# Kernel tuning notes

Measured on AMD Instinct MI355X. Metric: run time of the kernel, lower is better.

## Reference

```python
import jax, jax.numpy as jnp
import numpy as np

NUM_STAGES = 4
NUM_CODEBOOKS = 1024  # 2**vq_bitrate_per_stage
DATA_DIM = 256
BEAM = 4
N = 4096
EPS = 1e-12


def setup_inputs() -> dict:
    key = jax.random.key(0)
    k1, k2, k3 = jax.random.split(key, 3)
    x = jax.random.normal(k1, (N, DATA_DIM), jnp.float32)
    # codebooks initialized Uniform(-1/K, 1/K) as in torch __init__
    cb = jax.random.uniform(k2, (NUM_STAGES * NUM_CODEBOOKS, DATA_DIM), jnp.float32,
                            -1.0 / NUM_CODEBOOKS, 1.0 / NUM_CODEBOOKS)
    rv = jax.random.normal(k3, (N, DATA_DIM), jnp.float32)
    return {"input_data": x, "codebooks": cb, "random_vector": rv, "train_mode": 1}


def _beam_search(x, codebooks):
    """Returns best_tuples [N, S]: per-sample global codebook indices, one per stage slot."""
    B, D = x.shape
    S, K, W = NUM_STAGES, NUM_CODEBOOKS, BEAM
    cb2 = jnp.sum(codebooks ** 2, axis=1)  # [S*K]

    def dists(q):  # [..., D] -> [..., S*K] squared euclidean
        return jnp.sum(q ** 2, axis=-1, keepdims=True) - 2.0 * (q @ codebooks.T) + cb2

    stage_of = jnp.arange(S * K) // K  # stage id of each flat codebook row

    # stage 0: top-BEAM nearest entries over all stages
    idx0 = jax.lax.top_k(-dists(x), W)[1].astype(jnp.int32)  # [B, W]
    tuples = jnp.full((B, W, S), -1, jnp.int32).at[:, :, 0].set(idx0)

    for it in range(S - 1):
        # Faithful to source: vq_and_remainder loop subtracts codebooks[tuples[:,:,it]]
        # (it+1) times (the loop passes iter_number, not i).
        c_it = codebooks[tuples[:, :, it]]                      # [B, W, D]
        remainder = x[:, None, :] - (it + 1) * c_it             # [B, W, D]
        # stages already used by each beam (mask via NaN-codebooks in source == +inf here)
        used = tuples[:, :, :it + 1] // K                       # [B, W, it+1]
        banned = (used[:, :, :, None] == jnp.arange(S)).any(axis=2)  # [B, W, S]
        d = dists(remainder)                                    # [B, W, S*K]
        d = jnp.where(banned[:, :, stage_of], jnp.inf, d)
        cand = jax.lax.top_k(-d, W)[1].astype(jnp.int32)        # [B, W, W]
        prime = jnp.repeat(tuples[:, :, None, :], W, axis=2)    # [B, W, W, S]
        prime = prime.at[:, :, :, it + 1].set(cand).reshape(B, W * W, S)
        # mse over the (it+2) filled slots
        q = jnp.sum(codebooks[prime[:, :, :it + 2]], axis=2)    # [B, W*W, D]
        mse = jnp.mean((x[:, None, :] - q) ** 2, axis=2)        # [B, W*W]
        if it < S - 2:
            sel = jax.lax.top_k(-mse, W)[1]                     # [B, W] smallest-mse beams
            tuples = jnp.take_along_axis(prime, sel[:, :, None], axis=1)
        else:
            best = jnp.argmin(mse, axis=1)                      # [B]
            return jnp.take_along_axis(prime, best[:, None, None], axis=1)[:, 0, :]


def reference(input_data, codebooks, random_vector, train_mode):
    best = _beam_search(input_data, jax.lax.stop_gradient(codebooks))  # [N, S] int32
    quantized = jnp.sum(codebooks[best], axis=1)                       # [N, D]
    # noise substitution VQ
    nh = jnp.sqrt(jnp.sum((input_data - quantized) ** 2, axis=1, keepdims=True))
    nr = jnp.sqrt(jnp.sum(random_vector ** 2, axis=1, keepdims=True))
    nsvq = input_data + (nh / nr + EPS) * random_vector
    # codebooks_used starts at zero; +=1 at unique selected indices -> usage indicator
    used = jnp.zeros(NUM_STAGES * NUM_CODEBOOKS, jnp.int32).at[best.reshape(-1)].set(1)
    used = used.reshape(NUM_STAGES, NUM_CODEBOOKS)
    if train_mode:
        return (nsvq, used)
    return (quantized, used)
```

## Files before the change

kernel.cpp:

```cpp
#include <hip/hip_runtime.h>
#include <math.h>

#define NSTAGES 4
#define NCB     1024
#define SK      4096
#define D       256
#define BEAM_W  4
#define NB      4096
#define INFF    __builtin_huge_valf()
#define RB      128
#define CBL     256
#define BK      32
#define NCBLK   (SK / CBL)

typedef unsigned long long u64;


template <typename F>
__device__ __forceinline__ float xw84(F v) {
  float r[32];
#pragma unroll
  for (int l = 0; l < 32; ++l) r[l] = v(l);
  for (int i = 32; i < 256; i += 32)
#pragma unroll
    for (int l = 0; l < 32; ++l) r[l] = __fadd_rn(r[l], v(i + l));
  float w[8];
#pragma unroll
  for (int j = 0; j < 8; ++j)
    w[j] = __fadd_rn(__fadd_rn(__fadd_rn(r[j], r[8 + j]), r[16 + j]), r[24 + j]);
  float s0 = __fadd_rn(w[0], w[4]);
  float s1 = __fadd_rn(w[1], w[5]);
  float s2 = __fadd_rn(w[2], w[6]);
  float s3 = __fadd_rn(w[3], w[7]);
  float t0 = __fadd_rn(s0, s2);
  float t1 = __fadd_rn(s1, s3);
  return __fadd_rn(t0, t1);
}

__device__ __forceinline__ void ins4u(u64 v, u64 b[4]) {
  if (v < b[3]) {
    b[3] = v;
    if (b[3] < b[2]) { u64 t = b[2]; b[2] = b[3]; b[3] = t; }
    if (b[2] < b[1]) { u64 t = b[1]; b[1] = b[2]; b[2] = t; }
    if (b[1] < b[0]) { u64 t = b[0]; b[0] = b[1]; b[1] = t; }
  }
}

__device__ __forceinline__ u64 shflx64(u64 v, int m) {
  int lo = __shfl_xor((int)(unsigned)(v & 0xFFFFFFFFULL), m, 64);
  int hi = __shfl_xor((int)(unsigned)(v >> 32), m, 64);
  return ((u64)(unsigned)hi << 32) | (u64)(unsigned)lo;
}

__global__ __launch_bounds__(256) void cb2_pw(const float* __restrict__ cb,
                                              float* __restrict__ cb2) {
  int row = blockIdx.x * 256 + threadIdx.x;
  if (row >= SK) return;
  const float* c = cb + (size_t)row * D;
  cb2[row] = xw84([&](int d) { float t = c[d]; return __fmul_rn(t, t); });
}

__global__ __launch_bounds__(256) void s0_pw(const float* __restrict__ x,
                                             float* __restrict__ Srow) {
  int row = blockIdx.x * 256 + threadIdx.x;
  if (row >= NB) return;
  const float* xr = x + (size_t)row * D;
  Srow[row] = xw84([&](int d) { float t = xr[d]; return __fmul_rn(t, t); });
}

__global__ __launch_bounds__(256) void srow_pw(const float* __restrict__ x,
                                               const float* __restrict__ cb,
                                               const int* __restrict__ tuples,
                                               int it,
                                               float* __restrict__ Srow) {
  int row = blockIdx.x * 256 + threadIdx.x;
  if (row >= NB * BEAM_W) return;
  int s = row >> 2;
  int slot = tuples[row * NSTAGES + it];
  const float* xr = x + (size_t)s * D;
  const float* cr = cb + (size_t)slot * D;
  const float mf = (float)(it + 1);
  Srow[row] = xw84([&](int d) {
    float t = __fsub_rn(xr[d], __fmul_rn(mf, cr[d]));
    return __fmul_rn(t, t);
  });
}

__global__ __launch_bounds__(256) void transpose_rem(
    const float* __restrict__ x, const float* __restrict__ cbk,
    const int* __restrict__ tuples, int it, int isStep0, int nrows,
    float* __restrict__ AT) {
  __shared__ float tile[64][65];
  const int t = threadIdx.x;
  const int r0 = blockIdx.x * 64;
  const int d0 = blockIdx.y * 64;
  const float mf = (float)(it + 1);
  {
    int r = r0 + (t & 63);
    int db = (t >> 6) * 16;
    const float* xr;
    const float* cr = nullptr;
    if (isStep0) {
      xr = x + (size_t)r * D;
    } else {
      xr = x + (size_t)(r >> 2) * D;
      cr = cbk + (size_t)tuples[r * NSTAGES + it] * D;
    }
#pragma unroll
    for (int l = 0; l < 4; ++l) {
      float4 v = *(const float4*)&xr[d0 + db + l * 4];
      if (!isStep0) {
        float4 c = *(const float4*)&cr[d0 + db + l * 4];
        v.x = __fsub_rn(v.x, __fmul_rn(mf, c.x));
        v.y = __fsub_rn(v.y, __fmul_rn(mf, c.y));
        v.z = __fsub_rn(v.z, __fmul_rn(mf, c.z));
        v.w = __fsub_rn(v.w, __fmul_rn(mf, c.w));
      }
      tile[t & 63][db + l * 4 + 0] = v.x;
      tile[t & 63][db + l * 4 + 1] = v.y;
      tile[t & 63][db + l * 4 + 2] = v.z;
      tile[t & 63][db + l * 4 + 3] = v.w;
    }
  }
  __syncthreads();
  {
    int dd = t >> 2;
    int rb = (t & 3) * 16;
    float* orow = AT + (size_t)(d0 + dd) * nrows + r0 + rb;
#pragma unroll
    for (int l = 0; l < 4; ++l) {
      float4 v = make_float4(tile[rb + l * 4 + 0][dd], tile[rb + l * 4 + 1][dd],
                             tile[rb + l * 4 + 2][dd], tile[rb + l * 4 + 3][dd]);
      *(float4*)&orow[l * 4] = v;
    }
  }
}

__global__ __launch_bounds__(256, 2) void gemm_plain(
    const float* __restrict__ AT, const float* __restrict__ BT, int nrows,
    float* __restrict__ Gout) {
  __shared__ __align__(16) float AsF[BK * 128];
  __shared__ __align__(16) float BsF[BK * 256];
  const int tid  = threadIdx.x;
  const int wv   = tid >> 6;
  const int lane = tid & 63;
  const int tx = tid & 15, ty = tid >> 4;
  const int row0 = blockIdx.y * RB;
  const int col0 = blockIdx.x * CBL;

  const float* aSrc[4];
  const float* bSrc[8];
#pragma unroll
  for (int c = 0; c < 4; ++c) {
    int f = (wv * 4 + c) * 256 + lane * 4;
    aSrc[c] = AT + (size_t)(f >> 7) * nrows + row0 + (f & 127);
  }
#pragma unroll
  for (int c = 0; c < 8; ++c) {
    int f = (wv * 8 + c) * 256 + lane * 4;
    bSrc[c] = BT + (size_t)(f >> 8) * SK + col0 + (f & 255);
  }

  float acc[8][16];
#pragma unroll
  for (int i = 0; i < 8; ++i)
#pragma unroll
    for (int j = 0; j < 16; ++j) acc[i][j] = 0.0f;

  for (int kt = 0; kt < D; kt += BK) {
#pragma unroll
    for (int c = 0; c < 4; ++c)
      __builtin_amdgcn_global_load_lds(
          (const __attribute__((address_space(1))) void*)aSrc[c],
          (__attribute__((address_space(3))) void*)(AsF + (wv * 4 + c) * 256), 16, 0, 0);
#pragma unroll
    for (int c = 0; c < 8; ++c)
      __builtin_amdgcn_global_load_lds(
          (const __attribute__((address_space(1))) void*)bSrc[c],
          (__attribute__((address_space(3))) void*)(BsF + (wv * 8 + c) * 256), 16, 0, 0);
#pragma unroll
    for (int c = 0; c < 4; ++c) aSrc[c] += (size_t)BK * nrows;
#pragma unroll
    for (int c = 0; c < 8; ++c) bSrc[c] += (size_t)BK * SK;
    __syncthreads();

#pragma unroll 8
    for (int k = 0; k < BK; ++k) {
      float a[8], b[16];
      *(float4*)&a[0]  = *(const float4*)&AsF[k * 128 + ty * 4];
      *(float4*)&a[4]  = *(const float4*)&AsF[k * 128 + 64 + ty * 4];
      *(float4*)&b[0]  = *(const float4*)&BsF[k * 256 + tx * 4];
      *(float4*)&b[4]  = *(const float4*)&BsF[k * 256 + 64 + tx * 4];
      *(float4*)&b[8]  = *(const float4*)&BsF[k * 256 + 128 + tx * 4];
      *(float4*)&b[12] = *(const float4*)&BsF[k * 256 + 192 + tx * 4];
#pragma unroll
      for (int i = 0; i < 8; ++i)
#pragma unroll
        for (int j = 0; j < 16; ++j)
          acc[i][j] = __fmaf_rn(a[i], b[j], acc[i][j]);
    }
    __syncthreads();
  }

#pragma unroll
  for (int i = 0; i < 8; ++i) {
    int lrow = (i & 3) + ((i >> 2) * 64) + ty * 4;
    float* go = Gout + (size_t)(row0 + lrow) * SK + col0;
#pragma unroll
    for (int jj = 0; jj < 4; ++jj) {
      float4 v = make_float4(acc[i][jj * 4 + 0], acc[i][jj * 4 + 1],
                             acc[i][jj * 4 + 2], acc[i][jj * 4 + 3]);
      *(float4*)&go[jj * 64 + tx * 4] = v;
    }
  }
}

__global__ __launch_bounds__(256) void beam_full(
    const float* __restrict__ XC, const float* __restrict__ G,
    const float* __restrict__ Srow0, const float* __restrict__ cb2,
    const float* __restrict__ x, const float* __restrict__ cb,
    int* __restrict__ best) {
  const int s = blockIdx.x;
  const int t = threadIdx.x;
  const int b = t >> 6, l = t & 63;
  __shared__ float xcs[SK];
  __shared__ int   tup_s[4][NSTAGES];
  __shared__ float msek[16];
  __shared__ int   primes[16][NSTAGES];

  for (int i = t; i < SK / 4; i += 256)
    *(float4*)&xcs[i * 4] = *(const float4*)&XC[(size_t)s * SK + i * 4];
  __syncthreads();

  {
    const float S0 = Srow0[s];
    u64 b4[4] = {~0ULL, ~0ULL, ~0ULL, ~0ULL};
#pragma unroll 4
    for (int i = 0; i < 16; ++i) {
      int j = (i * 64 + l) * 4;
      float4 x4 = *(const float4*)&xcs[j];
      float4 c4 = *(const float4*)&cb2[j];
      float k0 = __fadd_rn(__fsub_rn(S0, __fmul_rn(2.0f, x4.x)), c4.x);
      float k1 = __fadd_rn(__fsub_rn(S0, __fmul_rn(2.0f, x4.y)), c4.y);
      float k2 = __fadd_rn(__fsub_rn(S0, __fmul_rn(2.0f, x4.z)), c4.z);
      float k3 = __fadd_rn(__fsub_rn(S0, __fmul_rn(2.0f, x4.w)), c4.w);
      ins4u(((u64)__float_as_uint(k0) << 32) | (unsigned)(j + 0), b4);
      ins4u(((u64)__float_as_uint(k1) << 32) | (unsigned)(j + 1), b4);
      ins4u(((u64)__float_as_uint(k2) << 32) | (unsigned)(j + 2), b4);
      ins4u(((u64)__float_as_uint(k3) << 32) | (unsigned)(j + 3), b4);
    }
#pragma unroll
    for (int m = 1; m < 64; m <<= 1) {
      u64 o0 = shflx64(b4[0], m);
      u64 o1 = shflx64(b4[1], m);
      u64 o2 = shflx64(b4[2], m);
      u64 o3 = shflx64(b4[3], m);
      ins4u(o0, b4);
      ins4u(o1, b4);
      ins4u(o2, b4);
      ins4u(o3, b4);
    }
    if (l == 0) tup_s[b][0] = (int)(b4[b] & 0xFFFFFFFFULL);
  }
  __syncthreads();

  for (int it = 0; it < NSTAGES - 1; ++it) {
    const float mf = (float)(it + 1);
    const int slot = tup_s[b][it];
    int banned = 0;
    for (int a = 0; a <= it; ++a) banned |= 1 << (tup_s[b][a] >> 10);

    float S;
    {
      const int ll = l & 31;
      const float* xr = x + (size_t)s * D;
      const float* cr = cb + (size_t)slot * D;
      float tt = __fsub_rn(xr[ll], __fmul_rn(mf, cr[ll]));
      float rl = __fmul_rn(tt, tt);
      for (int i = 32; i < 256; i += 32) {
        float t2 = __fsub_rn(xr[ll + i], __fmul_rn(mf, cr[ll + i]));
        rl = __fadd_rn(rl, __fmul_rn(t2, t2));
      }
      int j = l & 7;
      float rj   = __shfl(rl, j, 64);
      float rj8  = __shfl(rl, j + 8, 64);
      float rj16 = __shfl(rl, j + 16, 64);
      float rj24 = __shfl(rl, j + 24, 64);
      float w = __fadd_rn(__fadd_rn(__fadd_rn(rj, rj8), rj16), rj24);
      float w0 = __shfl(w, 0, 64), w1 = __shfl(w, 1, 64);
      float w2 = __shfl(w, 2, 64), w3 = __shfl(w, 3, 64);
      float w4 = __shfl(w, 4, 64), w5 = __shfl(w, 5, 64);
      float w6 = __shfl(w, 6, 64), w7 = __shfl(w, 7, 64);
      float s0 = __fadd_rn(w0, w4);
      float s1 = __fadd_rn(w1, w5);
      float s2 = __fadd_rn(w2, w6);
      float s3 = __fadd_rn(w3, w7);
      float t0 = __fadd_rn(s0, s2);
      float t1 = __fadd_rn(s1, s3);
      S = __fadd_rn(t0, t1);
    }

    const float* gr = G + (size_t)slot * SK;

    u64 b4[4] = {~0ULL, ~0ULL, ~0ULL, ~0ULL};
#pragma unroll 4
    for (int i = 0; i < 16; ++i) {
      int j = (i * 64 + l) * 4;
      float4 g4 = *(const float4*)&gr[j];
      float4 x4 = *(const float4*)&xcs[j];
      float4 c4 = *(const float4*)&cb2[j];
      int ban = (banned >> (j >> 10)) & 1;
      float m0 = __fsub_rn(x4.x, __fmul_rn(mf, g4.x));
      float m1 = __fsub_rn(x4.y, __fmul_rn(mf, g4.y));
      float m2 = __fsub_rn(x4.z, __fmul_rn(mf, g4.z));
      float m3 = __fsub_rn(x4.w, __fmul_rn(mf, g4.w));
      float k0 = ban ? INFF : __fadd_rn(__fsub_rn(S, __fmul_rn(2.0f, m0)), c4.x);
      float k1 = ban ? INFF : __fadd_rn(__fsub_rn(S, __fmul_rn(2.0f, m1)), c4.y);
      float k2 = ban ? INFF : __fadd_rn(__fsub_rn(S, __fmul_rn(2.0f, m2)), c4.z);
      float k3 = ban ? INFF : __fadd_rn(__fsub_rn(S, __fmul_rn(2.0f, m3)), c4.w);
      ins4u(((u64)__float_as_uint(k0) << 32) | (unsigned)(j + 0), b4);
      ins4u(((u64)__float_as_uint(k1) << 32) | (unsigned)(j + 1), b4);
      ins4u(((u64)__float_as_uint(k2) << 32) | (unsigned)(j + 2), b4);
      ins4u(((u64)__float_as_uint(k3) << 32) | (unsigned)(j + 3), b4);
    }
#pragma unroll
    for (int m = 1; m < 64; m <<= 1) {
      u64 o0 = shflx64(b4[0], m);
      u64 o1 = shflx64(b4[1], m);
      u64 o2 = shflx64(b4[2], m);
      u64 o3 = shflx64(b4[3], m);
      ins4u(o0, b4);
      ins4u(o1, b4);
      ins4u(o2, b4);
      ins4u(o3, b4);
    }

    {
      const int L = it + 2;
#pragma unroll
      for (int pi = 0; pi < 4; ++pi) {
        const int p = b * 4 + pi;
        int tpl[NSTAGES];
        for (int a = 0; a < NSTAGES; ++a) tpl[a] = tup_s[b][a];
        tpl[it + 1] = (int)(b4[pi] & 0xFFFFFFFFULL);
        if (l == 0)
          for (int a = 0; a < NSTAGES; ++a) primes[p][a] = tpl[a];
        float v[4];
#pragma unroll
        for (int m = 0; m < 4; ++m) {
          int d = l + m * 64;
          float q = cb[(size_t)tpl[0] * D + d];
          for (int a = 1; a < L; ++a) q = __fadd_rn(q, cb[(size_t)tpl[a] * D + d]);
          float dv = __fsub_rn(x[(size_t)s * D + d], q);
          v[m] = __fmul_rn(dv, dv);
        }
        float u0 = __shfl_xor(v[0], 32, 64);
        float u1 = __shfl_xor(v[1], 32, 64);
        float u2 = __shfl_xor(v[2], 32, 64);
        float u3 = __shfl_xor(v[3], 32, 64);
        float r0 = __fadd_rn(v[0], u0);
        r0 = __fadd_rn(r0, v[1]);
        r0 = __fadd_rn(r0, u1);
        r0 = __fadd_rn(r0, v[2]);
        r0 = __fadd_rn(r0, u2);
        r0 = __fadd_rn(r0, v[3]);
        r0 = __fadd_rn(r0, u3);
        float a8  = __shfl(r0, l + 8, 64);
        float a16 = __shfl(r0, l + 16, 64);
        float a24 = __shfl(r0, l + 24, 64);
        float w = __fadd_rn(__fadd_rn(__fadd_rn(r0, a8), a16), a24);
        float w0 = __shfl(w, 0, 64), w1 = __shfl(w, 1, 64);
        float w2 = __shfl(w, 2, 64), w3 = __shfl(w, 3, 64);
        float w4 = __shfl(w, 4, 64), w5 = __shfl(w, 5, 64);
        float w6 = __shfl(w, 6, 64), w7 = __shfl(w, 7, 64);
        float s0 = __fadd_rn(w0, w4);
        float s1 = __fadd_rn(w1, w5);
        float s2 = __fadd_rn(w2, w6);
        float s3 = __fadd_rn(w3, w7);
        float t0 = __fadd_rn(s0, s2);
        float t1 = __fadd_rn(s1, s3);
        float S2 = __fadd_rn(t0, t1);
        if (l == 0) msek[p] = __fmul_rn(S2, 0.00390625f);
      }
    }
    __syncthreads();

    if (t == 0) {
      if (it < NSTAGES - 2) {
        bool taken[16] = {false};
        int  newt[BEAM_W][NSTAGES];
        for (int rr2 = 0; rr2 < BEAM_W; ++rr2) {
          int bp = -1; float bk = 0.0f;
          for (int p = 0; p < 16; ++p) {
            if (taken[p]) continue;
            if (bp < 0 || msek[p] < bk) { bk = msek[p]; bp = p; }
          }
          taken[bp] = true;
          for (int a = 0; a < NSTAGES; ++a) newt[rr2][a] = primes[bp][a];
        }
        for (int rr2 = 0; rr2 < BEAM_W; ++rr2)
          for (int a = 0; a < NSTAGES; ++a) tup_s[rr2][a] = newt[rr2][a];
      } else {
        int bp = 0; float bk = msek[0];
        for (int p = 1; p < 16; ++p)
          if (msek[p] < bk) { bk = msek[p]; bp = p; }
        for (int a = 0; a < NSTAGES; ++a) best[s * NSTAGES + a] = primes[bp][a];
      }
    }
    __syncthreads();
  }
}

__global__ __launch_bounds__(256, 2) void gemm_fused(
    const float* __restrict__ AT, const float* __restrict__ BT,
    const float* __restrict__ Srow, const float* __restrict__ cb2,
    const int* __restrict__ tuples, int it, int isStep0, int nrows,
    u64* __restrict__ pki, float* __restrict__ XCout) {
  __shared__ __align__(16) char smem[66560];
  float* AsF = (float*)smem;
  float* BsF = (float*)(smem + 16384);
  u64*   tki = (u64*)smem;
  const int tid  = threadIdx.x;
  const int wv   = tid >> 6;
  const int lane = tid & 63;
  const int tx = tid & 15, ty = tid >> 4;
  const int row0 = blockIdx.y * RB;
  const int col0 = blockIdx.x * CBL;

  const float* aSrc[4];
  const float* bSrc[8];
#pragma unroll
  for (int c = 0; c < 4; ++c) {
    int f = (wv * 4 + c) * 256 + lane * 4;
    aSrc[c] = AT + (size_t)(f >> 7) * nrows + row0 + (f & 127);
  }
#pragma unroll
  for (int c = 0; c < 8; ++c) {
    int f = (wv * 8 + c) * 256 + lane * 4;
    bSrc[c] = BT + (size_t)(f >> 8) * SK + col0 + (f & 255);
  }

  float acc[8][16];
#pragma unroll
  for (int i = 0; i < 8; ++i)
#pragma unroll
    for (int j = 0; j < 16; ++j) acc[i][j] = 0.0f;

  for (int kt = 0; kt < D; kt += BK) {
#pragma unroll
    for (int c = 0; c < 4; ++c)
      __builtin_amdgcn_global_load_lds(
          (const __attribute__((address_space(1))) void*)aSrc[c],
          (__attribute__((address_space(3))) void*)(AsF + (wv * 4 + c) * 256), 16, 0, 0);
#pragma unroll
    for (int c = 0; c < 8; ++c)
      __builtin_amdgcn_global_load_lds(
          (const __attribute__((address_space(1))) void*)bSrc[c],
          (__attribute__((address_space(3))) void*)(BsF + (wv * 8 + c) * 256), 16, 0, 0);
#pragma unroll
    for (int c = 0; c < 4; ++c) aSrc[c] += (size_t)BK * nrows;
#pragma unroll
    for (int c = 0; c < 8; ++c) bSrc[c] += (size_t)BK * SK;
    __syncthreads();

#pragma unroll 8
    for (int k = 0; k < BK; ++k) {
      float a[8], b[16];
      *(float4*)&a[0]  = *(const float4*)&AsF[k * 128 + ty * 4];
      *(float4*)&a[4]  = *(const float4*)&AsF[k * 128 + 64 + ty * 4];
      *(float4*)&b[0]  = *(const float4*)&BsF[k * 256 + tx * 4];
      *(float4*)&b[4]  = *(const float4*)&BsF[k * 256 + 64 + tx * 4];
      *(float4*)&b[8]  = *(const float4*)&BsF[k * 256 + 128 + tx * 4];
      *(float4*)&b[12] = *(const float4*)&BsF[k * 256 + 192 + tx * 4];
#pragma unroll
      for (int i = 0; i < 8; ++i)
#pragma unroll
        for (int j = 0; j < 16; ++j)
          acc[i][j] = __fmaf_rn(a[i], b[j], acc[i][j]);
    }
    __syncthreads();
  }

  if (XCout) {
#pragma unroll
    for (int i = 0; i < 8; ++i) {
      int lrow = (i & 3) + ((i >> 2) * 64) + ty * 4;
      float* xo = XCout + (size_t)(row0 + lrow) * SK + col0;
#pragma unroll
      for (int jj = 0; jj < 4; ++jj) {
        float4 v = make_float4(acc[i][jj * 4 + 0], acc[i][jj * 4 + 1],
                               acc[i][jj * 4 + 2], acc[i][jj * 4 + 3]);
        *(float4*)&xo[(jj) * 64 + tx * 4] = v;
      }
    }
  }

#pragma unroll
  for (int i = 0; i < 8; ++i) {
    int lrow = (i & 3) + ((i >> 2) * 64) + ty * 4;
    int grow = row0 + lrow;
    float S = Srow[grow];
    int banned = 0;
    if (!isStep0)
      for (int a = 0; a <= it; ++a) banned |= 1 << (tuples[grow * NSTAGES + a] >> 10);
    u64 b4[4] = {~0ULL, ~0ULL, ~0ULL, ~0ULL};
#pragma unroll
    for (int j = 0; j < 16; ++j) {
      int gcol = col0 + (j & 3) + ((j >> 2) * 64) + tx * 4;
      float key = ((banned >> (gcol >> 10)) & 1)
                      ? INFF
                      : __fadd_rn(__fsub_rn(S, __fmul_rn(2.0f, acc[i][j])), cb2[gcol]);
      ins4u(((u64)__float_as_uint(key) << 32) | (unsigned)gcol, b4);
    }
#pragma unroll
    for (int s = 0; s < 4; ++s) tki[(size_t)lrow * 65 + tx * 4 + s] = b4[s];
  }
  __syncthreads();

  if (tid < RB) {
    u64 b4[4] = {~0ULL, ~0ULL, ~0ULL, ~0ULL};
    for (int t = 0; t < 16; ++t)
#pragma unroll
      for (int s = 0; s < 4; ++s) ins4u(tki[(size_t)tid * 65 + t * 4 + s], b4);
    size_t base = ((size_t)blockIdx.x * nrows + row0 + tid) * 4;
#pragma unroll
    for (int s = 0; s < 4; ++s) pki[base + s] = b4[s];
  }
}

__global__ __launch_bounds__(256) void reduce_top4(
    const u64* __restrict__ pki, int nrows, int isStep0,
    int* __restrict__ tup, int* __restrict__ cand) {
  int r = blockIdx.x * 256 + threadIdx.x;
  if (r >= nrows) return;
  u64 b4[4] = {~0ULL, ~0ULL, ~0ULL, ~0ULL};
  for (int cblk = 0; cblk < NCBLK; ++cblk) {
    size_t base = ((size_t)cblk * nrows + r) * 4;
    ins4u(pki[base + 0], b4);
    ins4u(pki[base + 1], b4);
    ins4u(pki[base + 2], b4);
    ins4u(pki[base + 3], b4);
  }
  if (isStep0) {
#pragma unroll
    for (int s = 0; s < 4; ++s)
      tup[(r * BEAM_W + s) * NSTAGES + 0] = (int)(b4[s] & 0xFFFFFFFFULL);
  } else {
#pragma unroll
    for (int s = 0; s < 4; ++s)
      cand[r * BEAM_W + s] = (int)(b4[s] & 0xFFFFFFFFULL);
  }
}

__global__ __launch_bounds__(256) void mse_select(const float* __restrict__ x,
                                                  const float* __restrict__ cb,
                                                  const int* __restrict__ cand,
                                                  int it,
                                                  int* __restrict__ tuples,
                                                  int* __restrict__ best) {
  const int s = blockIdx.x, tid = threadIdx.x;
  const int wv = tid >> 6, lane = tid & 63;
  __shared__ float buf[4][256];
  __shared__ float rr[4][32];
  __shared__ float msek[16];
  __shared__ int   primes[16][NSTAGES];
  const int L = it + 2;

  for (int pi = 0; pi < 4; ++pi) {
    const int p = wv * 4 + pi;
    const int b = p >> 2, c = p & 3;
    int tpl[NSTAGES];
    for (int a = 0; a < NSTAGES; ++a) tpl[a] = tuples[(s * BEAM_W + b) * NSTAGES + a];
    tpl[it + 1] = cand[(s * BEAM_W + b) * BEAM_W + c];
    if (lane == 0)
      for (int a = 0; a < NSTAGES; ++a) primes[p][a] = tpl[a];
    for (int d = lane; d < D; d += 64) {
      float q = cb[(size_t)tpl[0] * D + d];
      for (int a = 1; a < L; ++a) q = __fadd_rn(q, cb[(size_t)tpl[a] * D + d]);
      float v = __fsub_rn(x[(size_t)s * D + d], q);
      buf[wv][d] = __fmul_rn(v, v);
    }
    __syncthreads();
    if (lane < 32) {
      float r = buf[wv][lane];
      for (int i = 32; i < 256; i += 32) r = __fadd_rn(r, buf[wv][i + lane]);
      rr[wv][lane] = r;
    }
    __syncthreads();
    if (lane == 0) {
      float w[8];
#pragma unroll
      for (int j = 0; j < 8; ++j)
        w[j] = __fadd_rn(__fadd_rn(__fadd_rn(rr[wv][j], rr[wv][8 + j]), rr[wv][16 + j]),
                         rr[wv][24 + j]);
      float s0 = __fadd_rn(w[0], w[4]);
      float s1 = __fadd_rn(w[1], w[5]);
      float s2 = __fadd_rn(w[2], w[6]);
      float s3 = __fadd_rn(w[3], w[7]);
      float t0 = __fadd_rn(s0, s2);
      float t1 = __fadd_rn(s1, s3);
      float S2 = __fadd_rn(t0, t1);
      msek[p] = __fmul_rn(S2, 0.00390625f);
    }
    __syncthreads();
  }

  if (tid == 0) {
    if (it < NSTAGES - 2) {
      bool taken[16] = {false};
      int  newt[BEAM_W][NSTAGES];
      for (int r = 0; r < BEAM_W; ++r) {
        int bp = -1; float bk = 0.0f;
        for (int p = 0; p < 16; ++p) {
          if (taken[p]) continue;
          if (bp < 0 || msek[p] < bk) { bk = msek[p]; bp = p; }
        }
        taken[bp] = true;
        for (int a = 0; a < NSTAGES; ++a) newt[r][a] = primes[bp][a];
      }
      for (int r = 0; r < BEAM_W; ++r)
        for (int a = 0; a < NSTAGES; ++a) tuples[(s * BEAM_W + r) * NSTAGES + a] = newt[r][a];
    } else {
      int bp = 0; float bk = msek[0];
      for (int p = 1; p < 16; ++p)
        if (msek[p] < bk) { bk = msek[p]; bp = p; }
      for (int a = 0; a < NSTAGES; ++a) best[s * NSTAGES + a] = primes[bp][a];
    }
  }
}

__global__ void zero_used(float* __restrict__ u) {
  int t = blockIdx.x * 256 + threadIdx.x;
  if (t < SK) u[t] = 0.0f;
}

__global__ __launch_bounds__(256) void finalize_kernel(const float* __restrict__ x,
                                                       const float* __restrict__ cb,
                                                       const float* __restrict__ rvec,
                                                       const int* __restrict__ best,
                                                       const int* __restrict__ tmode,
                                                       float* __restrict__ out) {
  const int i = blockIdx.x;
  const int t = threadIdx.x;
  __shared__ double s1[256], s2[256];
  const int b0 = best[i * 4 + 0], b1 = best[i * 4 + 1];
  const int b2 = best[i * 4 + 2], b3 = best[i * 4 + 3];
  float q = ((cb[(size_t)b0 * D + t] + cb[(size_t)b1 * D + t]) + cb[(size_t)b2 * D + t]) +
            cb[(size_t)b3 * D + t];
  float xv = x[(size_t)i * D + t];
  float rv = rvec[(size_t)i * D + t];
  float df = xv - q;
  s1[t] = (double)df * (double)df;
  s2[t] = (double)rv * (double)rv;
  __syncthreads();
  for (int off = 128; off; off >>= 1) {
    if (t < off) { s1[t] += s1[t + off]; s2[t] += s2[t + off]; }
    __syncthreads();
  }
  float nh = sqrtf((float)s1[0]);
  float nr = sqrtf((float)s2[0]);
  float ratio = nh / nr + 1e-12f;
  out[(size_t)i * D + t] = (*tmode != 0) ? (xv + ratio * rv) : q;
  if (t < 4) out[(size_t)NB * D + best[i * 4 + t]] = 1.0f;
}

extern "C" void kernel_launch(void* const* d_in, const int* in_sizes, int n_in,
                              void* d_out, int out_size, void* d_ws, size_t ws_size,
                              hipStream_t stream) {
  const float* x   = (const float*)d_in[0];
  const float* cb  = (const float*)d_in[1];
  const float* rv  = (const float*)d_in[2];
  const int*   tm  = (const int*)d_in[3];
  float*       out = (float*)d_out;

  const size_t XC_BYTES    = (size_t)NB * SK * sizeof(float);
  const size_t G_BYTES     = (size_t)SK * SK * sizeof(float);
  const size_t BT_BYTES    = (size_t)D * SK * sizeof(float);
  const size_t AT0_BYTES   = (size_t)D * NB * sizeof(float);
  const size_t ATL_BYTES   = (size_t)D * NB * BEAM_W * sizeof(float);
  const size_t PKI0_BYTES  = (size_t)NCBLK * NB * BEAM_W * sizeof(u64);
  const size_t PKIL_BYTES  = (size_t)NCBLK * NB * BEAM_W * 4 * sizeof(u64);
  const size_t S_BYTES     = (size_t)NB * BEAM_W * sizeof(float);
  const size_t CB2_BYTES   = (size_t)SK * sizeof(float);
  const size_t TUP_BYTES   = (size_t)NB * BEAM_W * NSTAGES * sizeof(int);
  const size_t CAND_BYTES  = (size_t)NB * BEAM_W * BEAM_W * sizeof(int);
  const size_t BEST_BYTES  = (size_t)NB * NSTAGES * sizeof(int);
  const size_t SMALL = S_BYTES + CB2_BYTES + TUP_BYTES + CAND_BYTES + BEST_BYTES;

  const size_t NEW_TOTAL    = XC_BYTES + G_BYTES + BT_BYTES + AT0_BYTES + PKI0_BYTES + SMALL;
  const size_t LEGACY_TOTAL = PKIL_BYTES + BT_BYTES + ATL_BYTES + SMALL;

  if (ws_size >= NEW_TOTAL) {
    char* ws = (char*)d_ws;
    float* XC   = (float*)ws;  ws += XC_BYTES;
    float* G    = (float*)ws;  ws += G_BYTES;
    float* cbT  = (float*)ws;  ws += BT_BYTES;
    float* AT   = (float*)ws;  ws += AT0_BYTES;
    u64*   pki  = (u64*)ws;    ws += PKI0_BYTES;
    float* Srow = (float*)ws;  ws += S_BYTES;
    float* cb2  = (float*)ws;  ws += CB2_BYTES;
    int*   tup  = (int*)ws;    ws += TUP_BYTES;
    int*   cand = (int*)ws;    ws += CAND_BYTES;
    int*   best = (int*)ws;
    (void)pki; (void)cand;

    cb2_pw<<<SK / 256, 256, 0, stream>>>(cb, cb2);
    s0_pw<<<NB / 256, 256, 0, stream>>>(x, Srow);
    transpose_rem<<<dim3(SK / 64, D / 64), 256, 0, stream>>>(cb, cb, tup, 0, 1, SK, cbT);
    transpose_rem<<<dim3(NB / 64, D / 64), 256, 0, stream>>>(x, cb, tup, 0, 1, NB, AT);

    gemm_plain<<<dim3(NCBLK, SK / RB), 256, 0, stream>>>(cbT, cbT, SK, G);
    gemm_plain<<<dim3(NCBLK, NB / RB), 256, 0, stream>>>(AT, cbT, NB, XC);

    beam_full<<<NB, 256, 0, stream>>>(XC, G, Srow, cb2, x, cb, best);

    zero_used<<<SK / 256, 256, 0, stream>>>(out + (size_t)NB * D);
    finalize_kernel<<<NB, 256, 0, stream>>>(x, cb, rv, best, tm, out);
    return;
  }

  if (ws_size < LEGACY_TOTAL) return;
  char* ws = (char*)d_ws;
  u64*   pki  = (u64*)ws;    ws += PKIL_BYTES;
  float* cbT  = (float*)ws;  ws += BT_BYTES;
  float* AT   = (float*)ws;  ws += ATL_BYTES;
  float* Srow = (float*)ws;  ws += S_BYTES;
  float* cb2  = (float*)ws;  ws += CB2_BYTES;
  int*   tup  = (int*)ws;    ws += TUP_BYTES;
  int*   cand = (int*)ws;    ws += CAND_BYTES;
  int*   best = (int*)ws;

  cb2_pw<<<SK / 256, 256, 0, stream>>>(cb, cb2);
  s0_pw<<<NB / 256, 256, 0, stream>>>(x, Srow);
  transpose_rem<<<dim3(SK / 64, D / 64), 256, 0, stream>>>(cb, cb, tup, 0, 1, SK, cbT);
  transpose_rem<<<dim3(NB / 64, D / 64), 256, 0, stream>>>(x, cb, tup, 0, 1, NB, AT);

  gemm_fused<<<dim3(NCBLK, NB / RB), 256, 0, stream>>>(AT, cbT, Srow, cb2, tup, 0, 1, NB,
                                                       pki, nullptr);
  reduce_top4<<<NB / 256, 256, 0, stream>>>(pki, NB, 1, tup, cand);

  for (int it = 0; it < NSTAGES - 1; ++it) {
    srow_pw<<<(NB * BEAM_W) / 256, 256, 0, stream>>>(x, cb, tup, it, Srow);
    transpose_rem<<<dim3(NB * BEAM_W / 64, D / 64), 256, 0, stream>>>(x, cb, tup, it, 0,
                                                                      NB * BEAM_W, AT);
    gemm_fused<<<dim3(NCBLK, (NB * BEAM_W) / RB), 256, 0, stream>>>(
        AT, cbT, Srow, cb2, tup, it, 0, NB * BEAM_W, pki, nullptr);
    reduce_top4<<<(NB * BEAM_W) / 256, 256, 0, stream>>>(pki, NB * BEAM_W, 0, tup, cand);
    mse_select<<<NB, 256, 0, stream>>>(x, cb, cand, it, tup, best);
  }

  zero_used<<<SK / 256, 256, 0, stream>>>(out + (size_t)NB * D);
  finalize_kernel<<<NB, 256, 0, stream>>>(x, cb, rv, best, tm, out);
}
```

Baseline: 606.2 us.

## Fuse step-0 top-4 into XC GEMM and split beam scan across two waves

The step-0 nearest-codebook search moves out of the per-sample beam kernel into the XC GEMM epilogue, followed by a small cross-block reduce_top4 kernel. The beam kernel now runs 512 threads per sample, with two waves per beam each scanning half of the 4096 candidates. Their partial top-4 lists are merged through shared memory, and the MSE evaluation is split between the two waves. This raises parallelism in the serial per-sample phase, at the cost of an extra kernel launch, a pki workspace write/read, and an added block-wide sync per iteration.

```diff
diff --git a/kernel.cpp b/kernel.cpp
--- a/kernel.cpp
+++ b/kernel.cpp
@@ -215,53 +215,165 @@
   }
 }
 
-__global__ __launch_bounds__(256) void beam_full(
+__global__ __launch_bounds__(256, 2) void gemm_fused(
+    const float* __restrict__ AT, const float* __restrict__ BT,
+    const float* __restrict__ Srow, const float* __restrict__ cb2,
+    const int* __restrict__ tuples, int it, int isStep0, int nrows,
+    u64* __restrict__ pki, float* __restrict__ XCout) {
+  __shared__ __align__(16) char smem[66560];
+  float* AsF = (float*)smem;
+  float* BsF = (float*)(smem + 16384);
+  u64*   tki = (u64*)smem;
+  const int tid  = threadIdx.x;
+  const int wv   = tid >> 6;
+  const int lane = tid & 63;
+  const int tx = tid & 15, ty = tid >> 4;
+  const int row0 = blockIdx.y * RB;
+  const int col0 = blockIdx.x * CBL;
+
+  const float* aSrc[4];
+  const float* bSrc[8];
+#pragma unroll
+  for (int c = 0; c < 4; ++c) {
+    int f = (wv * 4 + c) * 256 + lane * 4;
+    aSrc[c] = AT + (size_t)(f >> 7) * nrows + row0 + (f & 127);
+  }
+#pragma unroll
+  for (int c = 0; c < 8; ++c) {
+    int f = (wv * 8 + c) * 256 + lane * 4;
+    bSrc[c] = BT + (size_t)(f >> 8) * SK + col0 + (f & 255);
+  }
+
+  float acc[8][16];
+#pragma unroll
+  for (int i = 0; i < 8; ++i)
+#pragma unroll
+    for (int j = 0; j < 16; ++j) acc[i][j] = 0.0f;
+
+  for (int kt = 0; kt < D; kt += BK) {
+#pragma unroll
+    for (int c = 0; c < 4; ++c)
+      __builtin_amdgcn_global_load_lds(
+          (const __attribute__((address_space(1))) void*)aSrc[c],
+          (__attribute__((address_space(3))) void*)(AsF + (wv * 4 + c) * 256), 16, 0, 0);
+#pragma unroll
+    for (int c = 0; c < 8; ++c)
+      __builtin_amdgcn_global_load_lds(
+          (const __attribute__((address_space(1))) void*)bSrc[c],
+          (__attribute__((address_space(3))) void*)(BsF + (wv * 8 + c) * 256), 16, 0, 0);
+#pragma unroll
+    for (int c = 0; c < 4; ++c) aSrc[c] += (size_t)BK * nrows;
+#pragma unroll
+    for (int c = 0; c < 8; ++c) bSrc[c] += (size_t)BK * SK;
+    __syncthreads();
+
+#pragma unroll 8
+    for (int k = 0; k < BK; ++k) {
+      float a[8], b[16];
+      *(float4*)&a[0]  = *(const float4*)&AsF[k * 128 + ty * 4];
+      *(float4*)&a[4]  = *(const float4*)&AsF[k * 128 + 64 + ty * 4];
+      *(float4*)&b[0]  = *(const float4*)&BsF[k * 256 + tx * 4];
+      *(float4*)&b[4]  = *(const float4*)&BsF[k * 256 + 64 + tx * 4];
+      *(float4*)&b[8]  = *(const float4*)&BsF[k * 256 + 128 + tx * 4];
+      *(float4*)&b[12] = *(const float4*)&BsF[k * 256 + 192 + tx * 4];
+#pragma unroll
+      for (int i = 0; i < 8; ++i)
+#pragma unroll
+        for (int j = 0; j < 16; ++j)
+          acc[i][j] = __fmaf_rn(a[i], b[j], acc[i][j]);
+    }
+    __syncthreads();
+  }
+
+  if (XCout) {
+#pragma unroll
+    for (int i = 0; i < 8; ++i) {
+      int lrow = (i & 3) + ((i >> 2) * 64) + ty * 4;
+      float* xo = XCout + (size_t)(row0 + lrow) * SK + col0;
+#pragma unroll
+      for (int jj = 0; jj < 4; ++jj) {
+        float4 v = make_float4(acc[i][jj * 4 + 0], acc[i][jj * 4 + 1],
+                               acc[i][jj * 4 + 2], acc[i][jj * 4 + 3]);
+        *(float4*)&xo[(jj) * 64 + tx * 4] = v;
+      }
+    }
+  }
+
+#pragma unroll
+  for (int i = 0; i < 8; ++i) {
+    int lrow = (i & 3) + ((i >> 2) * 64) + ty * 4;
+    int grow = row0 + lrow;
+    float S = Srow[grow];
+    int banned = 0;
+    if (!isStep0)
+      for (int a = 0; a <= it; ++a) banned |= 1 << (tuples[grow * NSTAGES + a] >> 10);
+    u64 b4[4] = {~0ULL, ~0ULL, ~0ULL, ~0ULL};
+#pragma unroll
+    for (int j = 0; j < 16; ++j) {
+      int gcol = col0 + (j & 3) + ((j >> 2) * 64) + tx * 4;
+      float key = ((banned >> (gcol >> 10)) & 1)
+                      ? INFF
+                      : __fadd_rn(__fsub_rn(S, __fmul_rn(2.0f, acc[i][j])), cb2[gcol]);
+      ins4u(((u64)__float_as_uint(key) << 32) | (unsigned)gcol, b4);
+    }
+#pragma unroll
+    for (int s = 0; s < 4; ++s) tki[(size_t)lrow * 65 + tx * 4 + s] = b4[s];
+  }
+  __syncthreads();
+
+  if (tid < RB) {
+    u64 b4[4] = {~0ULL, ~0ULL, ~0ULL, ~0ULL};
+    for (int t = 0; t < 16; ++t)
+#pragma unroll
+      for (int s = 0; s < 4; ++s) ins4u(tki[(size_t)tid * 65 + t * 4 + s], b4);
+    size_t base = ((size_t)blockIdx.x * nrows + row0 + tid) * 4;
+#pragma unroll
+    for (int s = 0; s < 4; ++s) pki[base + s] = b4[s];
+  }
+}
+
+__global__ __launch_bounds__(256) void reduce_top4(
+    const u64* __restrict__ pki, int nrows, int isStep0,
+    int* __restrict__ tup, int* __restrict__ cand) {
+  int r = blockIdx.x * 256 + threadIdx.x;
+  if (r >= nrows) return;
+  u64 b4[4] = {~0ULL, ~0ULL, ~0ULL, ~0ULL};
+  for (int cblk = 0; cblk < NCBLK; ++cblk) {
+    size_t base = ((size_t)cblk * nrows + r) * 4;
+    ins4u(pki[base + 0], b4);
+    ins4u(pki[base + 1], b4);
+    ins4u(pki[base + 2], b4);
+    ins4u(pki[base + 3], b4);
+  }
+  if (isStep0) {
+#pragma unroll
+    for (int s = 0; s < 4; ++s)
+      tup[(r * BEAM_W + s) * NSTAGES + 0] = (int)(b4[s] & 0xFFFFFFFFULL);
+  } else {
+#pragma unroll
+    for (int s = 0; s < 4; ++s)
+      cand[r * BEAM_W + s] = (int)(b4[s] & 0xFFFFFFFFULL);
+  }
+}
+
+__global__ __launch_bounds__(512) void beam_iter(
     const float* __restrict__ XC, const float* __restrict__ G,
-    const float* __restrict__ Srow0, const float* __restrict__ cb2,
+    const float* __restrict__ cb2,
     const float* __restrict__ x, const float* __restrict__ cb,
-    int* __restrict__ best) {
+    const int* __restrict__ tup0, int* __restrict__ best) {
   const int s = blockIdx.x;
   const int t = threadIdx.x;
-  const int b = t >> 6, l = t & 63;
+  const int wv = t >> 6, l = t & 63;
+  const int b = wv >> 1, half = wv & 1;
   __shared__ float xcs[SK];
   __shared__ int   tup_s[4][NSTAGES];
+  __shared__ u64   l2m[8][4];
   __shared__ float msek[16];
   __shared__ int   primes[16][NSTAGES];
 
-  for (int i = t; i < SK / 4; i += 256)
+  for (int i = t; i < SK / 4; i += 512)
     *(float4*)&xcs[i * 4] = *(const float4*)&XC[(size_t)s * SK + i * 4];
-  __syncthreads();
-
-  {
-    const float S0 = Srow0[s];
-    u64 b4[4] = {~0ULL, ~0ULL, ~0ULL, ~0ULL};
-#pragma unroll 4
-    for (int i = 0; i < 16; ++i) {
-      int j = (i * 64 + l) * 4;
-      float4 x4 = *(const float4*)&xcs[j];
-      float4 c4 = *(const float4*)&cb2[j];
-      float k0 = __fadd_rn(__fsub_rn(S0, __fmul_rn(2.0f, x4.x)), c4.x);
-      float k1 = __fadd_rn(__fsub_rn(S0, __fmul_rn(2.0f, x4.y)), c4.y);
-      float k2 = __fadd_rn(__fsub_rn(S0, __fmul_rn(2.0f, x4.z)), c4.z);
-      float k3 = __fadd_rn(__fsub_rn(S0, __fmul_rn(2.0f, x4.w)), c4.w);
-      ins4u(((u64)__float_as_uint(k0) << 32) | (unsigned)(j + 0), b4);
-      ins4u(((u64)__float_as_uint(k1) << 32) | (unsigned)(j + 1), b4);
-      ins4u(((u64)__float_as_uint(k2) << 32) | (unsigned)(j + 2), b4);
-      ins4u(((u64)__float_as_uint(k3) << 32) | (unsigned)(j + 3), b4);
-    }
-#pragma unroll
-    for (int m = 1; m < 64; m <<= 1) {
-      u64 o0 = shflx64(b4[0], m);
-      u64 o1 = shflx64(b4[1], m);
-      u64 o2 = shflx64(b4[2], m);
-      u64 o3 = shflx64(b4[3], m);
-      ins4u(o0, b4);
-      ins4u(o1, b4);
-      ins4u(o2, b4);
-      ins4u(o3, b4);
-    }
-    if (l == 0) tup_s[b][0] = (int)(b4[b] & 0xFFFFFFFFULL);
-  }
+  if (t < 16) tup_s[t >> 2][t & 3] = tup0[(s * BEAM_W + (t >> 2)) * NSTAGES + (t & 3)];
   __syncthreads();
 
   for (int it = 0; it < NSTAGES - 1; ++it) {
@@ -304,7 +416,7 @@
 
     u64 b4[4] = {~0ULL, ~0ULL, ~0ULL, ~0ULL};
 #pragma unroll 4
-    for (int i = 0; i < 16; ++i) {
+    for (int i = half * 8; i < half * 8 + 8; ++i) {
       int j = (i * 64 + l) * 4;
       float4 g4 = *(const float4*)&gr[j];
       float4 x4 = *(const float4*)&xcs[j];
@@ -334,15 +446,27 @@
       ins4u(o2, b4);
       ins4u(o3, b4);
     }
+    if (l == 0) {
+#pragma unroll
+      for (int k = 0; k < 4; ++k) l2m[wv][k] = b4[k];
+    }
+    __syncthreads();
+
+    u64 m4[4] = {~0ULL, ~0ULL, ~0ULL, ~0ULL};
+#pragma unroll
+    for (int k = 0; k < 4; ++k) ins4u(l2m[b * 2][k], m4);
+#pragma unroll
+    for (int k = 0; k < 4; ++k) ins4u(l2m[b * 2 + 1][k], m4);
 
     {
       const int L = it + 2;
 #pragma unroll
-      for (int pi = 0; pi < 4; ++pi) {
+      for (int pi2 = 0; pi2 < 2; ++pi2) {
+        const int pi = half * 2 + pi2;
         const int p = b * 4 + pi;
         int tpl[NSTAGES];
         for (int a = 0; a < NSTAGES; ++a) tpl[a] = tup_s[b][a];
-        tpl[it + 1] = (int)(b4[pi] & 0xFFFFFFFFULL);
+        tpl[it + 1] = (int)(m4[pi] & 0xFFFFFFFFULL);
         if (l == 0)
           for (int a = 0; a < NSTAGES; ++a) primes[p][a] = tpl[a];
         float v[4];
@@ -411,147 +535,6 @@
   }
 }
 
-__global__ __launch_bounds__(256, 2) void gemm_fused(
-    const float* __restrict__ AT, const float* __restrict__ BT,
-    const float* __restrict__ Srow, const float* __restrict__ cb2,
-    const int* __restrict__ tuples, int it, int isStep0, int nrows,
-    u64* __restrict__ pki, float* __restrict__ XCout) {
-  __shared__ __align__(16) char smem[66560];
-  float* AsF = (float*)smem;
-  float* BsF = (float*)(smem + 16384);
-  u64*   tki = (u64*)smem;
-  const int tid  = threadIdx.x;
-  const int wv   = tid >> 6;
-  const int lane = tid & 63;
-  const int tx = tid & 15, ty = tid >> 4;
-  const int row0 = blockIdx.y * RB;
-  const int col0 = blockIdx.x * CBL;
-
-  const float* aSrc[4];
-  const float* bSrc[8];
-#pragma unroll
-  for (int c = 0; c < 4; ++c) {
-    int f = (wv * 4 + c) * 256 + lane * 4;
-    aSrc[c] = AT + (size_t)(f >> 7) * nrows + row0 + (f & 127);
-  }
-#pragma unroll
-  for (int c = 0; c < 8; ++c) {
-    int f = (wv * 8 + c) * 256 + lane * 4;
-    bSrc[c] = BT + (size_t)(f >> 8) * SK + col0 + (f & 255);
-  }
-
-  float acc[8][16];
-#pragma unroll
-  for (int i = 0; i < 8; ++i)
-#pragma unroll
-    for (int j = 0; j < 16; ++j) acc[i][j] = 0.0f;
-
-  for (int kt = 0; kt < D; kt += BK) {
-#pragma unroll
-    for (int c = 0; c < 4; ++c)
-      __builtin_amdgcn_global_load_lds(
-          (const __attribute__((address_space(1))) void*)aSrc[c],
-          (__attribute__((address_space(3))) void*)(AsF + (wv * 4 + c) * 256), 16, 0, 0);
-#pragma unroll
-    for (int c = 0; c < 8; ++c)
-      __builtin_amdgcn_global_load_lds(
-          (const __attribute__((address_space(1))) void*)bSrc[c],
-          (__attribute__((address_space(3))) void*)(BsF + (wv * 8 + c) * 256), 16, 0, 0);
-#pragma unroll
-    for (int c = 0; c < 4; ++c) aSrc[c] += (size_t)BK * nrows;
-#pragma unroll
-    for (int c = 0; c < 8; ++c) bSrc[c] += (size_t)BK * SK;
-    __syncthreads();
-
-#pragma unroll 8
-    for (int k = 0; k < BK; ++k) {
-      float a[8], b[16];
-      *(float4*)&a[0]  = *(const float4*)&AsF[k * 128 + ty * 4];
-      *(float4*)&a[4]  = *(const float4*)&AsF[k * 128 + 64 + ty * 4];
-      *(float4*)&b[0]  = *(const float4*)&BsF[k * 256 + tx * 4];
-      *(float4*)&b[4]  = *(const float4*)&BsF[k * 256 + 64 + tx * 4];
-      *(float4*)&b[8]  = *(const float4*)&BsF[k * 256 + 128 + tx * 4];
-      *(float4*)&b[12] = *(const float4*)&BsF[k * 256 + 192 + tx * 4];
-#pragma unroll
-      for (int i = 0; i < 8; ++i)
-#pragma unroll
-        for (int j = 0; j < 16; ++j)
-          acc[i][j] = __fmaf_rn(a[i], b[j], acc[i][j]);
-    }
-    __syncthreads();
-  }
-
-  if (XCout) {
-#pragma unroll
-    for (int i = 0; i < 8; ++i) {
-      int lrow = (i & 3) + ((i >> 2) * 64) + ty * 4;
-      float* xo = XCout + (size_t)(row0 + lrow) * SK + col0;
-#pragma unroll
-      for (int jj = 0; jj < 4; ++jj) {
-        float4 v = make_float4(acc[i][jj * 4 + 0], acc[i][jj * 4 + 1],
-                               acc[i][jj * 4 + 2], acc[i][jj * 4 + 3]);
-        *(float4*)&xo[(jj) * 64 + tx * 4] = v;
-      }
-    }
-  }
-
-#pragma unroll
-  for (int i = 0; i < 8; ++i) {
-    int lrow = (i & 3) + ((i >> 2) * 64) + ty * 4;
-    int grow = row0 + lrow;
-    float S = Srow[grow];
-    int banned = 0;
-    if (!isStep0)
-      for (int a = 0; a <= it; ++a) banned |= 1 << (tuples[grow * NSTAGES + a] >> 10);
-    u64 b4[4] = {~0ULL, ~0ULL, ~0ULL, ~0ULL};
-#pragma unroll
-    for (int j = 0; j < 16; ++j) {
-      int gcol = col0 + (j & 3) + ((j >> 2) * 64) + tx * 4;
-      float key = ((banned >> (gcol >> 10)) & 1)
-                      ? INFF
-                      : __fadd_rn(__fsub_rn(S, __fmul_rn(2.0f, acc[i][j])), cb2[gcol]);
-      ins4u(((u64)__float_as_uint(key) << 32) | (unsigned)gcol, b4);
-    }
-#pragma unroll
-    for (int s = 0; s < 4; ++s) tki[(size_t)lrow * 65 + tx * 4 + s] = b4[s];
-  }
-  __syncthreads();
-
-  if (tid < RB) {
-    u64 b4[4] = {~0ULL, ~0ULL, ~0ULL, ~0ULL};
-    for (int t = 0; t < 16; ++t)
-#pragma unroll
-      for (int s = 0; s < 4; ++s) ins4u(tki[(size_t)tid * 65 + t * 4 + s], b4);
-    size_t base = ((size_t)blockIdx.x * nrows + row0 + tid) * 4;
-#pragma unroll
-    for (int s = 0; s < 4; ++s) pki[base + s] = b4[s];
-  }
-}
-
-__global__ __launch_bounds__(256) void reduce_top4(
-    const u64* __restrict__ pki, int nrows, int isStep0,
-    int* __restrict__ tup, int* __restrict__ cand) {
-  int r = blockIdx.x * 256 + threadIdx.x;
-  if (r >= nrows) return;
-  u64 b4[4] = {~0ULL, ~0ULL, ~0ULL, ~0ULL};
-  for (int cblk = 0; cblk < NCBLK; ++cblk) {
-    size_t base = ((size_t)cblk * nrows + r) * 4;
-    ins4u(pki[base + 0], b4);
-    ins4u(pki[base + 1], b4);
-    ins4u(pki[base + 2], b4);
-    ins4u(pki[base + 3], b4);
-  }
-  if (isStep0) {
-#pragma unroll
-    for (int s = 0; s < 4; ++s)
-      tup[(r * BEAM_W + s) * NSTAGES + 0] = (int)(b4[s] & 0xFFFFFFFFULL);
-  } else {
-#pragma unroll
-    for (int s = 0; s < 4; ++s)
-      cand[r * BEAM_W + s] = (int)(b4[s] & 0xFFFFFFFFULL);
-  }
-}
-
 __global__ __launch_bounds__(256) void mse_select(const float* __restrict__ x,
                                                   const float* __restrict__ cb,
                                                   const int* __restrict__ cand,
@@ -702,7 +685,6 @@
     int*   tup  = (int*)ws;    ws += TUP_BYTES;
     int*   cand = (int*)ws;    ws += CAND_BYTES;
     int*   best = (int*)ws;
-    (void)pki; (void)cand;
 
     cb2_pw<<<SK / 256, 256, 0, stream>>>(cb, cb2);
     s0_pw<<<NB / 256, 256, 0, stream>>>(x, Srow);
@@ -710,9 +692,11 @@
     transpose_rem<<<dim3(NB / 64, D / 64), 256, 0, stream>>>(x, cb, tup, 0, 1, NB, AT);
 
     gemm_plain<<<dim3(NCBLK, SK / RB), 256, 0, stream>>>(cbT, cbT, SK, G);
-    gemm_plain<<<dim3(NCBLK, NB / RB), 256, 0, stream>>>(AT, cbT, NB, XC);
-
-    beam_full<<<NB, 256, 0, stream>>>(XC, G, Srow, cb2, x, cb, best);
+    gemm_fused<<<dim3(NCBLK, NB / RB), 256, 0, stream>>>(AT, cbT, Srow, cb2, tup, 0, 1, NB,
+                                                         pki, XC);
+    reduce_top4<<<NB / 256, 256, 0, stream>>>(pki, NB, 1, tup, cand);
+
+    beam_iter<<<NB, 512, 0, stream>>>(XC, G, cb2, x, cb, tup, best);
 
     zero_used<<<SK / 256, 256, 0, stream>>>(out + (size_t)NB * D);
     finalize_kernel<<<NB, 256, 0, stream>>>(x, cb, rv, best, tm, out);
```

Result: slower. 749.9 us (+23.7%).
